# Kernel optimization log

Hardware: AMD Instinct MI355X
Metric: run time of the kernel (lower is better)

The kernel has to match this reference:

```python
import jax, jax.numpy as jnp
import numpy as np

NUM_ROIS = 333
EPS = 1e-5
SLOPE = 0.3  # LeakyReLU negative slope
BATCH = 512


def _make_meta():
    rng = np.random.RandomState(42)
    sizes = rng.randint(100, 501, NUM_ROIS)          # per-ROI input voxels
    reduced = np.maximum(sizes // 8, 8)              # per-ROI reduced dim
    return sizes, reduced


def setup_inputs() -> dict:
    sizes, reduced = _make_meta()
    total = int(sizes.sum())
    max_in = int(sizes.max())
    max_out = int(reduced.max())
    in_off = np.concatenate([[0], np.cumsum(sizes)])[:-1]
    # gather index [R, max_in]; out-of-range slots point at a zero pad column (= total)
    k = np.arange(max_in)
    idx = np.where(k[None, :] < sizes[:, None], in_off[:, None] + k[None, :], total)
    # map concat positions -> flattened [R*max_out] positions (drops per-ROI padding)
    src_index = np.concatenate([r * max_out + np.arange(reduced[r]) for r in range(NUM_ROIS)])
    concat_dim = int(reduced.sum())

    key = jax.random.key(0)
    ks = jax.random.split(key, 12)
    x = jax.random.normal(ks[0], (BATCH, total), jnp.float32)
    W_enc = jax.random.normal(ks[1], (NUM_ROIS, max_out, max_in), jnp.float32) * 0.05
    b_enc = jax.random.normal(ks[2], (NUM_ROIS, max_out), jnp.float32) * 0.02
    gamma = 1.0 + 0.1 * jax.random.normal(ks[3], (NUM_ROIS, max_out), jnp.float32)
    beta = 0.1 * jax.random.normal(ks[4], (NUM_ROIS, max_out), jnp.float32)
    run_mean = 0.1 * jax.random.normal(ks[5], (NUM_ROIS, max_out), jnp.float32)
    run_var = jax.random.uniform(ks[6], (NUM_ROIS, max_out), jnp.float32, 0.5, 1.5)
    W_reg = jax.random.normal(ks[7], (300, concat_dim), jnp.float32) * 0.02
    b_reg = jax.random.normal(ks[8], (300,), jnp.float32) * 0.02
    W_cls = jax.random.normal(ks[9], (180, 300), jnp.float32) * 0.05
    b_cls = jax.random.normal(ks[10], (180,), jnp.float32) * 0.02
    return {
        'x': x, 'W_enc': W_enc, 'b_enc': b_enc, 'gamma': gamma, 'beta': beta,
        'run_mean': run_mean, 'run_var': run_var,
        'W_reg': W_reg, 'b_reg': b_reg, 'W_cls': W_cls, 'b_cls': b_cls,
        'idx': jnp.asarray(idx, jnp.int32), 'src_index': jnp.asarray(src_index, jnp.int32),
    }


def reference(x, W_enc, b_enc, gamma, beta, run_mean, run_var,
              W_reg, b_reg, W_cls, b_cls, idx, src_index):
    B = x.shape[0]
    # pad a zero column so ragged gather lands on zeros; padded weight cols hit zeros
    x_pad = jnp.concatenate([x, jnp.zeros((B, 1), x.dtype)], axis=1)
    g = x_pad[:, idx]                                   # [B, R, max_in]
    z = jnp.einsum('brk,rok->bro', g, W_enc) + b_enc    # grouped GEMM: [B, R, max_out]
    # BatchNorm1d (inference form with running stats) + LeakyReLU(0.3)
    y = gamma * (z - run_mean) * jax.lax.rsqrt(run_var + EPS) + beta
    y = jnp.where(y > 0, y, SLOPE * y)
    concat_out = y.reshape(B, -1)[:, src_index]         # [B, concat_dim] (drop ROI padding)
    reg_out = concat_out @ W_reg.T + b_reg              # dropout is identity in eval
    y_pred = jax.nn.softmax(reg_out @ W_cls.T + b_cls, axis=-1)
    return concat_out, reg_out, y_pred
```

## Files before the change

kernel.cpp:

```cpp
#include <hip/hip_runtime.h>
#include <hip/hip_bf16.h>

#define NROIS 333
#define BATCH 512
#define NREG 300
#define NCLS 180
#define EPSV 1e-5f
#define SLOPEV 0.3f

typedef __attribute__((ext_vector_type(8))) short bf16x8;
typedef __attribute__((ext_vector_type(4))) float f32x4;

static __device__ __forceinline__ bf16x8 pack8(const float v[8]) {
  union { bf16x8 o; __hip_bfloat16 h[8]; } u;
  #pragma unroll
  for (int e = 0; e < 8; e++) u.h[e] = __float2bfloat16(v[e]);
  return u.o;
}

__global__ void meta_kernel(const int* __restrict__ idx, const int* __restrict__ src,
                            int* __restrict__ meta, int max_in, int max_out,
                            int total, int concat_dim) {
  int r = blockIdx.x * blockDim.x + threadIdx.x;
  if (r >= NROIS) return;
  const int* row = idx + (long)r * max_in;
  int in_off = row[0];
  int lo = 0, hi = max_in;
  while (lo < hi) { int mid = (lo + hi) >> 1; if (row[mid] < total) lo = mid + 1; else hi = mid; }
  int size = lo;
  int t1 = r * max_out;
  lo = 0; hi = concat_dim;
  while (lo < hi) { int mid = (lo + hi) >> 1; if (src[mid] < t1) lo = mid + 1; else hi = mid; }
  int out_off = lo;
  int t2 = t1 + max_out;
  hi = concat_dim;
  while (lo < hi) { int mid = (lo + hi) >> 1; if (src[mid] < t2) lo = mid + 1; else hi = mid; }
  meta[r] = in_off;
  meta[NROIS + r] = size;
  meta[2 * NROIS + r] = out_off;
  meta[3 * NROIS + r] = lo - out_off;
}

__global__ void init_reg_kernel(const float* __restrict__ b_reg, float* __restrict__ reg_out) {
  int i = blockIdx.x * blockDim.x + threadIdx.x;
  if (i < BATCH * NREG) reg_out[i] = b_reg[i % NREG];
}

__global__ __launch_bounds__(256) void enc_kernel(
    const float* __restrict__ x,
    const float* __restrict__ W_enc,
    const float* __restrict__ b_enc,
    const float* __restrict__ gamma,
    const float* __restrict__ beta,
    const float* __restrict__ run_mean,
    const float* __restrict__ run_var,
    const int* __restrict__ meta,
    float* __restrict__ concat_out,
    int total, int max_in, int max_out, int concat_dim) {
  int r = blockIdx.x;
  int b0 = blockIdx.y * 128;
  int in_off  = meta[r];
  int size    = meta[NROIS + r];
  int out_off = meta[2 * NROIS + r];
  int red     = meta[3 * NROIS + r];
  int ntiles  = (red + 15) >> 4;

  __shared__ __hip_bfloat16 xs[2][128 * 64];
  __shared__ __hip_bfloat16 wsh[2][64 * 64];

  int t = threadIdx.x;
  int rbase = t >> 3, chk = t & 7;
  const float* xg0 = x + (long)(b0 + rbase) * total + in_off;
  long xstride = (long)32 * total;
  const float* wg0 = W_enc + ((long)r * max_out + rbase) * max_in;
  long wstride = (long)32 * max_in;

  int w = t >> 6, l = t & 63, lq = l >> 4, lm = l & 15;

  f32x4 acc[2][4];
  #pragma unroll
  for (int i = 0; i < 2; i++)
    #pragma unroll
    for (int nb = 0; nb < 4; nb++) acc[i][nb] = (f32x4){0.f, 0.f, 0.f, 0.f};

  int nsteps = (size + 63) >> 6;
  float xr[4][8], wr[2][8];

  auto load_regs = [&](int kb) {
    int k0 = kb + chk * 8;
    if (k0 + 8 <= size) {
      #pragma unroll
      for (int s = 0; s < 4; s++) {
        const float* p = xg0 + (long)s * xstride + k0;
        float4 a = *(const float4*)p, b = *(const float4*)(p + 4);
        xr[s][0]=a.x; xr[s][1]=a.y; xr[s][2]=a.z; xr[s][3]=a.w;
        xr[s][4]=b.x; xr[s][5]=b.y; xr[s][6]=b.z; xr[s][7]=b.w;
      }
      #pragma unroll
      for (int s = 0; s < 2; s++) {
        if (rbase + 32 * s < red) {
          const float* p = wg0 + (long)s * wstride + k0;
          float4 a = *(const float4*)p, b = *(const float4*)(p + 4);
          wr[s][0]=a.x; wr[s][1]=a.y; wr[s][2]=a.z; wr[s][3]=a.w;
          wr[s][4]=b.x; wr[s][5]=b.y; wr[s][6]=b.z; wr[s][7]=b.w;
        } else {
          #pragma unroll
          for (int e = 0; e < 8; e++) wr[s][e] = 0.f;
        }
      }
    } else {
      #pragma unroll
      for (int s = 0; s < 4; s++)
        #pragma unroll
        for (int e = 0; e < 8; e++)
          xr[s][e] = (k0 + e < size) ? xg0[(long)s * xstride + k0 + e] : 0.f;
      #pragma unroll
      for (int s = 0; s < 2; s++) {
        bool rv = rbase + 32 * s < red;
        #pragma unroll
        for (int e = 0; e < 8; e++)
          wr[s][e] = (rv && k0 + e < size) ? wg0[(long)s * wstride + k0 + e] : 0.f;
      }
    }
  };
  auto write_lds = [&](int buf) {
    #pragma unroll
    for (int s = 0; s < 4; s++) {
      int row = rbase + 32 * s, cs = chk ^ (row & 7);
      *(bf16x8*)&xs[buf][(row * 8 + cs) * 8] = pack8(xr[s]);
    }
    #pragma unroll
    for (int s = 0; s < 2; s++) {
      int row = rbase + 32 * s, cs = chk ^ (row & 7);
      *(bf16x8*)&wsh[buf][(row * 8 + cs) * 8] = pack8(wr[s]);
    }
  };

  load_regs(0);
  write_lds(0);
  __syncthreads();

  for (int s = 0; s < nsteps; s++) {
    int buf = s & 1;
    bool more = (s + 1 < nsteps);
    if (more) load_regs((s + 1) * 64);
    #pragma unroll
    for (int kk = 0; kk < 2; kk++) {
      bf16x8 af[2];
      #pragma unroll
      for (int i = 0; i < 2; i++) {
        int row = 32 * w + 16 * i + lm, cs = (lq + 4 * kk) ^ (row & 7);
        af[i] = *(const bf16x8*)&xs[buf][(row * 8 + cs) * 8];
      }
      for (int nb = 0; nb < ntiles; nb++) {
        int row = 16 * nb + lm, cs = (lq + 4 * kk) ^ (row & 7);
        bf16x8 bfr = *(const bf16x8*)&wsh[buf][(row * 8 + cs) * 8];
        #pragma unroll
        for (int i = 0; i < 2; i++)
          acc[i][nb] = __builtin_amdgcn_mfma_f32_16x16x32_bf16(af[i], bfr, acc[i][nb], 0, 0, 0);
      }
    }
    if (more) write_lds(buf ^ 1);
    __syncthreads();
  }

  long base = (long)r * max_out;
  for (int nb = 0; nb < ntiles; nb++) {
    int oc = nb * 16 + lm;
    if (oc < red) {
      float sc  = gamma[base + oc] * rsqrtf(run_var[base + oc] + EPSV);
      float off = beta[base + oc] + sc * (b_enc[base + oc] - run_mean[base + oc]);
      #pragma unroll
      for (int i = 0; i < 2; i++) {
        #pragma unroll
        for (int j = 0; j < 4; j++) {
          int br = b0 + 32 * w + 16 * i + lq * 4 + j;
          float y = sc * acc[i][nb][j] + off;
          y = (y > 0.f) ? y : SLOPEV * y;
          concat_out[(long)br * concat_dim + out_off + oc] = y;
        }
      }
    }
  }
}

__global__ __launch_bounds__(256) void reg_kernel(
    const float* __restrict__ concat,
    const float* __restrict__ W_reg,
    float* __restrict__ reg_out,
    int concat_dim, int span) {
  int j0 = blockIdx.x * 64;
  int b0 = blockIdx.y * 128;
  int kstart = blockIdx.z * span;
  int kend = min(kstart + span, concat_dim);
  if (kstart >= kend) return;
  int ntiles = min(4, (NREG - j0 + 15) >> 4);
  int klen = kend - kstart;

  __shared__ __hip_bfloat16 as_[2][128 * 64];
  __shared__ __hip_bfloat16 bs_[2][64 * 64];

  int t = threadIdx.x;
  int rbase = t >> 3, chk = t & 7;
  const float* ag0 = concat + (long)(b0 + rbase) * concat_dim + kstart;
  long astride = (long)32 * concat_dim;
  const float* bg0 = W_reg + (long)(j0 + rbase) * concat_dim + kstart;
  long bstride = (long)32 * concat_dim;

  int w = t >> 6, l = t & 63, lq = l >> 4, lm = l & 15;

  f32x4 acc[2][4];
  #pragma unroll
  for (int i = 0; i < 2; i++)
    #pragma unroll
    for (int nb = 0; nb < 4; nb++) acc[i][nb] = (f32x4){0.f, 0.f, 0.f, 0.f};

  int nsteps = (klen + 63) >> 6;
  float ar[4][8], br[2][8];

  auto load_regs = [&](int kb) {
    int k0 = kb + chk * 8;
    if (k0 + 8 <= klen) {
      #pragma unroll
      for (int s = 0; s < 4; s++) {
        const float* p = ag0 + (long)s * astride + k0;
        float4 a = *(const float4*)p, b = *(const float4*)(p + 4);
        ar[s][0]=a.x; ar[s][1]=a.y; ar[s][2]=a.z; ar[s][3]=a.w;
        ar[s][4]=b.x; ar[s][5]=b.y; ar[s][6]=b.z; ar[s][7]=b.w;
      }
      #pragma unroll
      for (int s = 0; s < 2; s++) {
        if (j0 + rbase + 32 * s < NREG) {
          const float* p = bg0 + (long)s * bstride + k0;
          float4 a = *(const float4*)p, b = *(const float4*)(p + 4);
          br[s][0]=a.x; br[s][1]=a.y; br[s][2]=a.z; br[s][3]=a.w;
          br[s][4]=b.x; br[s][5]=b.y; br[s][6]=b.z; br[s][7]=b.w;
        } else {
          #pragma unroll
          for (int e = 0; e < 8; e++) br[s][e] = 0.f;
        }
      }
    } else {
      #pragma unroll
      for (int s = 0; s < 4; s++)
        #pragma unroll
        for (int e = 0; e < 8; e++)
          ar[s][e] = (k0 + e < klen) ? ag0[(long)s * astride + k0 + e] : 0.f;
      #pragma unroll
      for (int s = 0; s < 2; s++) {
        bool rv = j0 + rbase + 32 * s < NREG;
        #pragma unroll
        for (int e = 0; e < 8; e++)
          br[s][e] = (rv && k0 + e < klen) ? bg0[(long)s * bstride + k0 + e] : 0.f;
      }
    }
  };
  auto write_lds = [&](int buf) {
    #pragma unroll
    for (int s = 0; s < 4; s++) {
      int row = rbase + 32 * s, cs = chk ^ (row & 7);
      *(bf16x8*)&as_[buf][(row * 8 + cs) * 8] = pack8(ar[s]);
    }
    #pragma unroll
    for (int s = 0; s < 2; s++) {
      int row = rbase + 32 * s, cs = chk ^ (row & 7);
      *(bf16x8*)&bs_[buf][(row * 8 + cs) * 8] = pack8(br[s]);
    }
  };

  load_regs(0);
  write_lds(0);
  __syncthreads();

  for (int s = 0; s < nsteps; s++) {
    int buf = s & 1;
    bool more = (s + 1 < nsteps);
    if (more) load_regs((s + 1) * 64);
    #pragma unroll
    for (int kk = 0; kk < 2; kk++) {
      bf16x8 af[2];
      #pragma unroll
      for (int i = 0; i < 2; i++) {
        int row = 32 * w + 16 * i + lm, cs = (lq + 4 * kk) ^ (row & 7);
        af[i] = *(const bf16x8*)&as_[buf][(row * 8 + cs) * 8];
      }
      for (int nb = 0; nb < ntiles; nb++) {
        int row = 16 * nb + lm, cs = (lq + 4 * kk) ^ (row & 7);
        bf16x8 bfr = *(const bf16x8*)&bs_[buf][(row * 8 + cs) * 8];
        #pragma unroll
        for (int i = 0; i < 2; i++)
          acc[i][nb] = __builtin_amdgcn_mfma_f32_16x16x32_bf16(af[i], bfr, acc[i][nb], 0, 0, 0);
      }
    }
    if (more) write_lds(buf ^ 1);
    __syncthreads();
  }

  for (int nb = 0; nb < ntiles; nb++) {
    int j = j0 + nb * 16 + lm;
    if (j < NREG) {
      #pragma unroll
      for (int i = 0; i < 2; i++)
        #pragma unroll
        for (int jj = 0; jj < 4; jj++) {
          int br2 = b0 + 32 * w + 16 * i + lq * 4 + jj;
          atomicAdd(&reg_out[(long)br2 * NREG + j], acc[i][nb][jj]);
        }
    }
  }
}

__global__ __launch_bounds__(192) void cls_kernel(
    const float* __restrict__ reg_out,
    const float* __restrict__ W_cls,
    const float* __restrict__ b_cls,
    float* __restrict__ cls_out) {
  int b = blockIdx.x;
  int t = threadIdx.x;
  __shared__ __align__(16) float rrow[NREG];
  __shared__ float lm[3];
  for (int iB = t; iB < NREG; iB += 192) rrow[iB] = reg_out[(long)b * NREG + iB];
  __syncthreads();
  float s = 0.f;
  if (t < NCLS) {
    s = b_cls[t];
    const float4* wr  = (const float4*)(W_cls + (long)t * NREG);
    const float4* rr4 = (const float4*)rrow;
    #pragma unroll 5
    for (int i = 0; i < NREG / 4; ++i) {
      float4 wv = wr[i], rv = rr4[i];
      s += wv.x * rv.x + wv.y * rv.y + wv.z * rv.z + wv.w * rv.w;
    }
  }
  float v = (t < NCLS) ? s : -3.4e38f;
  #pragma unroll
  for (int o = 32; o > 0; o >>= 1) v = fmaxf(v, __shfl_xor(v, o, 64));
  if ((t & 63) == 0) lm[t >> 6] = v;
  __syncthreads();
  float bmax = fmaxf(fmaxf(lm[0], lm[1]), lm[2]);
  __syncthreads();
  float e = (t < NCLS) ? __expf(s - bmax) : 0.f;
  float ss = e;
  #pragma unroll
  for (int o = 32; o > 0; o >>= 1) ss += __shfl_xor(ss, o, 64);
  if ((t & 63) == 0) lm[t >> 6] = ss;
  __syncthreads();
  float bsum = lm[0] + lm[1] + lm[2];
  if (t < NCLS) cls_out[(long)b * NCLS + t] = e / bsum;
}

extern "C" void kernel_launch(void* const* d_in, const int* in_sizes, int n_in,
                              void* d_out, int out_size, void* d_ws, size_t ws_size,
                              hipStream_t stream) {
  const float* x     = (const float*)d_in[0];
  const float* W_enc = (const float*)d_in[1];
  const float* b_enc = (const float*)d_in[2];
  const float* gam   = (const float*)d_in[3];
  const float* bet   = (const float*)d_in[4];
  const float* rmean = (const float*)d_in[5];
  const float* rvar  = (const float*)d_in[6];
  const float* W_reg = (const float*)d_in[7];
  const float* b_reg = (const float*)d_in[8];
  const float* W_cls = (const float*)d_in[9];
  const float* b_cls = (const float*)d_in[10];
  const int* idx = (const int*)d_in[11];
  const int* src = (const int*)d_in[12];

  int total      = in_sizes[0] / BATCH;
  int max_out    = in_sizes[2] / NROIS;
  int max_in     = in_sizes[11] / NROIS;
  int concat_dim = in_sizes[12];

  int* meta = (int*)d_ws;

  float* out_concat = (float*)d_out;
  float* out_reg = out_concat + (long)BATCH * concat_dim;
  float* out_cls = out_reg + (long)BATCH * NREG;

  meta_kernel<<<dim3((NROIS + 255) / 256), 256, 0, stream>>>(idx, src, meta, max_in, max_out, total, concat_dim);
  init_reg_kernel<<<dim3((BATCH * NREG + 255) / 256), 256, 0, stream>>>(b_reg, out_reg);
  enc_kernel<<<dim3(NROIS, BATCH / 128), 256, 0, stream>>>(x, W_enc, b_enc, gam, bet, rmean, rvar,
                                                           meta, out_concat, total, max_in, max_out, concat_dim);
  const int SPAN = 448;
  int nsplit = (concat_dim + SPAN - 1) / SPAN;
  reg_kernel<<<dim3((NREG + 63) / 64, BATCH / 128, nsplit), 256, 0, stream>>>(out_concat, W_reg, out_reg, concat_dim, SPAN);
  cls_kernel<<<BATCH, 192, 0, stream>>>(out_reg, W_cls, b_cls, out_cls);
}
```

Baseline: 471.8 us.

## Shrink GEMM K-step to 32, pad LDS rows, pre-convert reg GEMM operands to bf16

The encoder and regression GEMMs now use a K-step of 32 with padded 40-element LDS rows in place of XOR swizzling, and each thread loads a single W row. This drops the predicated zero-fill for W rows beyond the reduced dimension by clamping the row index. A new transcode kernel converts concat_out and W_reg to bf16 in workspace so the regression GEMM reads half the bytes. The regression split-K is fixed at 32 splits. The cost is an extra pass over concat_out and W_reg, more split-K atomics, and twice as many barriers per unit of K.

```diff
diff --git a/kernel.cpp b/kernel.cpp
--- a/kernel.cpp
+++ b/kernel.cpp
@@ -46,6 +46,27 @@
   if (i < BATCH * NREG) reg_out[i] = b_reg[i % NREG];
 }
 
+__global__ __launch_bounds__(256) void transcode_kernel(
+    const float* __restrict__ concat, const float* __restrict__ W_reg,
+    __hip_bfloat16* __restrict__ cbf, __hip_bfloat16* __restrict__ wbf,
+    int cd, int cdp) {
+  int row = blockIdx.x;
+  const float* src;
+  __hip_bfloat16* dst;
+  if (row < BATCH) { src = concat + (long)row * cd; dst = cbf + (long)row * cdp; }
+  else             { src = W_reg + (long)(row - BATCH) * cd; dst = wbf + (long)(row - BATCH) * cdp; }
+  for (int k = threadIdx.x * 8; k < cdp; k += 256 * 8) {
+    if (k + 8 <= cd) {
+      float4 a = *(const float4*)(src + k), b = *(const float4*)(src + k + 4);
+      float v[8] = {a.x, a.y, a.z, a.w, b.x, b.y, b.z, b.w};
+      *(bf16x8*)(dst + k) = pack8(v);
+    } else {
+      for (int e = 0; e < 8 && k + e < cdp; e++)
+        dst[k + e] = __float2bfloat16((k + e < cd) ? src[k + e] : 0.f);
+    }
+  }
+}
+
 __global__ __launch_bounds__(256) void enc_kernel(
     const float* __restrict__ x,
     const float* __restrict__ W_enc,
@@ -65,15 +86,15 @@
   int red     = meta[3 * NROIS + r];
   int ntiles  = (red + 15) >> 4;
 
-  __shared__ __hip_bfloat16 xs[2][128 * 64];
-  __shared__ __hip_bfloat16 wsh[2][64 * 64];
+  __shared__ __hip_bfloat16 xs[2][128][40];
+  __shared__ __hip_bfloat16 wsh[2][64][40];
 
   int t = threadIdx.x;
-  int rbase = t >> 3, chk = t & 7;
-  const float* xg0 = x + (long)(b0 + rbase) * total + in_off;
-  long xstride = (long)32 * total;
-  const float* wg0 = W_enc + ((long)r * max_out + rbase) * max_in;
-  long wstride = (long)32 * max_in;
+  int row0 = t >> 2, chk = t & 3;
+  const float* xg0 = x + (long)(b0 + row0) * total + in_off;
+  long xstride = (long)64 * total;
+  int wrow = (row0 < red) ? row0 : (red - 1);
+  const float* wg0 = W_enc + ((long)r * max_out + wrow) * max_in;
 
   int w = t >> 6, l = t & 63, lq = l >> 4, lm = l & 15;
 
@@ -83,57 +104,39 @@
     #pragma unroll
     for (int nb = 0; nb < 4; nb++) acc[i][nb] = (f32x4){0.f, 0.f, 0.f, 0.f};
 
-  int nsteps = (size + 63) >> 6;
-  float xr[4][8], wr[2][8];
+  int nsteps = (size + 31) >> 5;
+  float xr[2][8], wr[8];
 
   auto load_regs = [&](int kb) {
     int k0 = kb + chk * 8;
     if (k0 + 8 <= size) {
       #pragma unroll
-      for (int s = 0; s < 4; s++) {
+      for (int s = 0; s < 2; s++) {
         const float* p = xg0 + (long)s * xstride + k0;
         float4 a = *(const float4*)p, b = *(const float4*)(p + 4);
         xr[s][0]=a.x; xr[s][1]=a.y; xr[s][2]=a.z; xr[s][3]=a.w;
         xr[s][4]=b.x; xr[s][5]=b.y; xr[s][6]=b.z; xr[s][7]=b.w;
       }
-      #pragma unroll
-      for (int s = 0; s < 2; s++) {
-        if (rbase + 32 * s < red) {
-          const float* p = wg0 + (long)s * wstride + k0;
-          float4 a = *(const float4*)p, b = *(const float4*)(p + 4);
-          wr[s][0]=a.x; wr[s][1]=a.y; wr[s][2]=a.z; wr[s][3]=a.w;
-          wr[s][4]=b.x; wr[s][5]=b.y; wr[s][6]=b.z; wr[s][7]=b.w;
-        } else {
-          #pragma unroll
-          for (int e = 0; e < 8; e++) wr[s][e] = 0.f;
-        }
-      }
+      const float* p = wg0 + k0;
+      float4 a = *(const float4*)p, b = *(const float4*)(p + 4);
+      wr[0]=a.x; wr[1]=a.y; wr[2]=a.z; wr[3]=a.w;
+      wr[4]=b.x; wr[5]=b.y; wr[6]=b.z; wr[7]=b.w;
     } else {
       #pragma unroll
-      for (int s = 0; s < 4; s++)
+      for (int s = 0; s < 2; s++)
         #pragma unroll
         for (int e = 0; e < 8; e++)
           xr[s][e] = (k0 + e < size) ? xg0[(long)s * xstride + k0 + e] : 0.f;
       #pragma unroll
-      for (int s = 0; s < 2; s++) {
-        bool rv = rbase + 32 * s < red;
-        #pragma unroll
-        for (int e = 0; e < 8; e++)
-          wr[s][e] = (rv && k0 + e < size) ? wg0[(long)s * wstride + k0 + e] : 0.f;
-      }
+      for (int e = 0; e < 8; e++)
+        wr[e] = (k0 + e < size) ? wg0[k0 + e] : 0.f;
     }
   };
   auto write_lds = [&](int buf) {
     #pragma unroll
-    for (int s = 0; s < 4; s++) {
-      int row = rbase + 32 * s, cs = chk ^ (row & 7);
-      *(bf16x8*)&xs[buf][(row * 8 + cs) * 8] = pack8(xr[s]);
-    }
-    #pragma unroll
-    for (int s = 0; s < 2; s++) {
-      int row = rbase + 32 * s, cs = chk ^ (row & 7);
-      *(bf16x8*)&wsh[buf][(row * 8 + cs) * 8] = pack8(wr[s]);
-    }
+    for (int s = 0; s < 2; s++)
+      *(bf16x8*)&xs[buf][row0 + 64 * s][chk * 8] = pack8(xr[s]);
+    *(bf16x8*)&wsh[buf][row0][chk * 8] = pack8(wr);
   };
 
   load_regs(0);
@@ -143,22 +146,16 @@
   for (int s = 0; s < nsteps; s++) {
     int buf = s & 1;
     bool more = (s + 1 < nsteps);
-    if (more) load_regs((s + 1) * 64);
-    #pragma unroll
-    for (int kk = 0; kk < 2; kk++) {
-      bf16x8 af[2];
-      #pragma unroll
-      for (int i = 0; i < 2; i++) {
-        int row = 32 * w + 16 * i + lm, cs = (lq + 4 * kk) ^ (row & 7);
-        af[i] = *(const bf16x8*)&xs[buf][(row * 8 + cs) * 8];
-      }
-      for (int nb = 0; nb < ntiles; nb++) {
-        int row = 16 * nb + lm, cs = (lq + 4 * kk) ^ (row & 7);
-        bf16x8 bfr = *(const bf16x8*)&wsh[buf][(row * 8 + cs) * 8];
-        #pragma unroll
-        for (int i = 0; i < 2; i++)
-          acc[i][nb] = __builtin_amdgcn_mfma_f32_16x16x32_bf16(af[i], bfr, acc[i][nb], 0, 0, 0);
-      }
+    if (more) load_regs((s + 1) * 32);
+    bf16x8 af[2];
+    #pragma unroll
+    for (int i = 0; i < 2; i++)
+      af[i] = *(const bf16x8*)&xs[buf][32 * w + 16 * i + lm][lq * 8];
+    for (int nb = 0; nb < ntiles; nb++) {
+      bf16x8 bfr = *(const bf16x8*)&wsh[buf][16 * nb + lm][lq * 8];
+      #pragma unroll
+      for (int i = 0; i < 2; i++)
+        acc[i][nb] = __builtin_amdgcn_mfma_f32_16x16x32_bf16(af[i], bfr, acc[i][nb], 0, 0, 0);
     }
     if (more) write_lds(buf ^ 1);
     __syncthreads();
@@ -184,29 +181,31 @@
   }
 }
 
+template <bool BF>
 __global__ __launch_bounds__(256) void reg_kernel(
-    const float* __restrict__ concat,
-    const float* __restrict__ W_reg,
-    float* __restrict__ reg_out,
-    int concat_dim, int span) {
+    const void* __restrict__ Asrc, const void* __restrict__ Bsrc,
+    float* __restrict__ reg_out, int cd, int astride, int span) {
   int j0 = blockIdx.x * 64;
   int b0 = blockIdx.y * 128;
   int kstart = blockIdx.z * span;
-  int kend = min(kstart + span, concat_dim);
+  int kend = min(kstart + span, cd);
   if (kstart >= kend) return;
   int ntiles = min(4, (NREG - j0 + 15) >> 4);
+
+  __shared__ __hip_bfloat16 as_[2][128][40];
+  __shared__ __hip_bfloat16 bs_[2][64][40];
+
+  int t = threadIdx.x;
+  int row0 = t >> 2, chk = t & 3;
+  int jr = j0 + row0;
+  int bj = (jr < NREG) ? jr : (NREG - 1);
+  const __hip_bfloat16* aB = (const __hip_bfloat16*)Asrc + (long)(b0 + row0) * astride + kstart;
+  const __hip_bfloat16* bB = (const __hip_bfloat16*)Bsrc + (long)bj * astride + kstart;
+  const float* aF = (const float*)Asrc + (long)(b0 + row0) * astride + kstart;
+  const float* bF = (const float*)Bsrc + (long)bj * astride + kstart;
+  long astr = (long)64 * astride;
   int klen = kend - kstart;
 
-  __shared__ __hip_bfloat16 as_[2][128 * 64];
-  __shared__ __hip_bfloat16 bs_[2][64 * 64];
-
-  int t = threadIdx.x;
-  int rbase = t >> 3, chk = t & 7;
-  const float* ag0 = concat + (long)(b0 + rbase) * concat_dim + kstart;
-  long astride = (long)32 * concat_dim;
-  const float* bg0 = W_reg + (long)(j0 + rbase) * concat_dim + kstart;
-  long bstride = (long)32 * concat_dim;
-
   int w = t >> 6, l = t & 63, lq = l >> 4, lm = l & 15;
 
   f32x4 acc[2][4];
@@ -215,57 +214,54 @@
     #pragma unroll
     for (int nb = 0; nb < 4; nb++) acc[i][nb] = (f32x4){0.f, 0.f, 0.f, 0.f};
 
-  int nsteps = (klen + 63) >> 6;
-  float ar[4][8], br[2][8];
+  int nsteps = (klen + 31) >> 5;
+  bf16x8 arv[2], brv;
+  float arf[2][8], brf[8];
 
   auto load_regs = [&](int kb) {
     int k0 = kb + chk * 8;
     if (k0 + 8 <= klen) {
-      #pragma unroll
-      for (int s = 0; s < 4; s++) {
-        const float* p = ag0 + (long)s * astride + k0;
+      if (BF) {
+        #pragma unroll
+        for (int s = 0; s < 2; s++) arv[s] = *(const bf16x8*)(aB + (long)s * astr + k0);
+        brv = *(const bf16x8*)(bB + k0);
+      } else {
+        #pragma unroll
+        for (int s = 0; s < 2; s++) {
+          const float* p = aF + (long)s * astr + k0;
+          float4 a = *(const float4*)p, b = *(const float4*)(p + 4);
+          arf[s][0]=a.x; arf[s][1]=a.y; arf[s][2]=a.z; arf[s][3]=a.w;
+          arf[s][4]=b.x; arf[s][5]=b.y; arf[s][6]=b.z; arf[s][7]=b.w;
+        }
+        const float* p = bF + k0;
         float4 a = *(const float4*)p, b = *(const float4*)(p + 4);
-        ar[s][0]=a.x; ar[s][1]=a.y; ar[s][2]=a.z; ar[s][3]=a.w;
-        ar[s][4]=b.x; ar[s][5]=b.y; ar[s][6]=b.z; ar[s][7]=b.w;
-      }
-      #pragma unroll
-      for (int s = 0; s < 2; s++) {
-        if (j0 + rbase + 32 * s < NREG) {
-          const float* p = bg0 + (long)s * bstride + k0;
-          float4 a = *(const float4*)p, b = *(const float4*)(p + 4);
-          br[s][0]=a.x; br[s][1]=a.y; br[s][2]=a.z; br[s][3]=a.w;
-          br[s][4]=b.x; br[s][5]=b.y; br[s][6]=b.z; br[s][7]=b.w;
-        } else {
-          #pragma unroll
-          for (int e = 0; e < 8; e++) br[s][e] = 0.f;
-        }
+        brf[0]=a.x; brf[1]=a.y; brf[2]=a.z; brf[3]=a.w;
+        brf[4]=b.x; brf[5]=b.y; brf[6]=b.z; brf[7]=b.w;
       }
     } else {
-      #pragma unroll
-      for (int s = 0; s < 4; s++)
-        #pragma unroll
-        for (int e = 0; e < 8; e++)
-          ar[s][e] = (k0 + e < klen) ? ag0[(long)s * astride + k0 + e] : 0.f;
-      #pragma unroll
-      for (int s = 0; s < 2; s++) {
-        bool rv = j0 + rbase + 32 * s < NREG;
-        #pragma unroll
-        for (int e = 0; e < 8; e++)
-          br[s][e] = (rv && k0 + e < klen) ? bg0[(long)s * bstride + k0 + e] : 0.f;
+      union { bf16x8 v; __hip_bfloat16 h[8]; } ua[2], ub;
+      #pragma unroll
+      for (int s = 0; s < 2; s++)
+        #pragma unroll
+        for (int e = 0; e < 8; e++) {
+          bool in = (k0 + e < klen);
+          if (BF) ua[s].h[e] = in ? aB[(long)s * astr + k0 + e] : __float2bfloat16(0.f);
+          else    arf[s][e] = in ? aF[(long)s * astr + k0 + e] : 0.f;
+        }
+      #pragma unroll
+      for (int e = 0; e < 8; e++) {
+        bool in = (k0 + e < klen);
+        if (BF) ub.h[e] = in ? bB[k0 + e] : __float2bfloat16(0.f);
+        else    brf[e] = in ? bF[k0 + e] : 0.f;
       }
+      if (BF) { arv[0] = ua[0].v; arv[1] = ua[1].v; brv = ub.v; }
     }
   };
   auto write_lds = [&](int buf) {
     #pragma unroll
-    for (int s = 0; s < 4; s++) {
-      int row = rbase + 32 * s, cs = chk ^ (row & 7);
-      *(bf16x8*)&as_[buf][(row * 8 + cs) * 8] = pack8(ar[s]);
-    }
-    #pragma unroll
-    for (int s = 0; s < 2; s++) {
-      int row = rbase + 32 * s, cs = chk ^ (row & 7);
-      *(bf16x8*)&bs_[buf][(row * 8 + cs) * 8] = pack8(br[s]);
-    }
+    for (int s = 0; s < 2; s++)
+      *(bf16x8*)&as_[buf][row0 + 64 * s][chk * 8] = BF ? arv[s] : pack8(arf[s]);
+    *(bf16x8*)&bs_[buf][row0][chk * 8] = BF ? brv : pack8(brf);
   };
 
   load_regs(0);
@@ -275,22 +271,16 @@
   for (int s = 0; s < nsteps; s++) {
     int buf = s & 1;
     bool more = (s + 1 < nsteps);
-    if (more) load_regs((s + 1) * 64);
-    #pragma unroll
-    for (int kk = 0; kk < 2; kk++) {
-      bf16x8 af[2];
-      #pragma unroll
-      for (int i = 0; i < 2; i++) {
-        int row = 32 * w + 16 * i + lm, cs = (lq + 4 * kk) ^ (row & 7);
-        af[i] = *(const bf16x8*)&as_[buf][(row * 8 + cs) * 8];
-      }
-      for (int nb = 0; nb < ntiles; nb++) {
-        int row = 16 * nb + lm, cs = (lq + 4 * kk) ^ (row & 7);
-        bf16x8 bfr = *(const bf16x8*)&bs_[buf][(row * 8 + cs) * 8];
-        #pragma unroll
-        for (int i = 0; i < 2; i++)
-          acc[i][nb] = __builtin_amdgcn_mfma_f32_16x16x32_bf16(af[i], bfr, acc[i][nb], 0, 0, 0);
-      }
+    if (more) load_regs((s + 1) * 32);
+    bf16x8 af[2];
+    #pragma unroll
+    for (int i = 0; i < 2; i++)
+      af[i] = *(const bf16x8*)&as_[buf][32 * w + 16 * i + lm][lq * 8];
+    for (int nb = 0; nb < ntiles; nb++) {
+      bf16x8 bfr = *(const bf16x8*)&bs_[buf][16 * nb + lm][lq * 8];
+      #pragma unroll
+      for (int i = 0; i < 2; i++)
+        acc[i][nb] = __builtin_amdgcn_mfma_f32_16x16x32_bf16(af[i], bfr, acc[i][nb], 0, 0, 0);
     }
     if (more) write_lds(buf ^ 1);
     __syncthreads();
@@ -370,8 +360,15 @@
   int max_out    = in_sizes[2] / NROIS;
   int max_in     = in_sizes[11] / NROIS;
   int concat_dim = in_sizes[12];
+  int cdp        = (concat_dim + 7) & ~7;
 
   int* meta = (int*)d_ws;
+  size_t bf_off = 8192;
+  size_t cbf_bytes = (size_t)BATCH * cdp * sizeof(__hip_bfloat16);
+  size_t wbf_bytes = (size_t)NREG * cdp * sizeof(__hip_bfloat16);
+  int use_bf = (ws_size >= bf_off + cbf_bytes + wbf_bytes) ? 1 : 0;
+  __hip_bfloat16* cbf = (__hip_bfloat16*)((char*)d_ws + bf_off);
+  __hip_bfloat16* wbf = (__hip_bfloat16*)((char*)d_ws + bf_off + cbf_bytes);
 
   float* out_concat = (float*)d_out;
   float* out_reg = out_concat + (long)BATCH * concat_dim;
@@ -381,8 +378,14 @@
   init_reg_kernel<<<dim3((BATCH * NREG + 255) / 256), 256, 0, stream>>>(b_reg, out_reg);
   enc_kernel<<<dim3(NROIS, BATCH / 128), 256, 0, stream>>>(x, W_enc, b_enc, gam, bet, rmean, rvar,
                                                            meta, out_concat, total, max_in, max_out, concat_dim);
-  const int SPAN = 448;
-  int nsplit = (concat_dim + SPAN - 1) / SPAN;
-  reg_kernel<<<dim3((NREG + 63) / 64, BATCH / 128, nsplit), 256, 0, stream>>>(out_concat, W_reg, out_reg, concat_dim, SPAN);
+  const int SPLIT = 32;
+  int span = ((concat_dim + SPLIT * 32 - 1) / (SPLIT * 32)) * 32;
+  dim3 rgrid((NREG + 63) / 64, BATCH / 128, SPLIT);
+  if (use_bf) {
+    transcode_kernel<<<BATCH + NREG, 256, 0, stream>>>(out_concat, W_reg, cbf, wbf, concat_dim, cdp);
+    reg_kernel<true><<<rgrid, 256, 0, stream>>>(cbf, wbf, out_reg, concat_dim, cdp, span);
+  } else {
+    reg_kernel<false><<<rgrid, 256, 0, stream>>>(out_concat, W_reg, out_reg, concat_dim, concat_dim, span);
+  }
   cls_kernel<<<BATCH, 192, 0, stream>>>(out_reg, W_cls, b_cls, out_cls);
 }
```

Result: no change. 473.4 us (+0.3%).
